# Optimization experiments

Measured on AMD Instinct MI355X. Metric: run time of the kernel, lower is better.

The kernel has to match this reference:

```python
import jax, jax.numpy as jnp
import numpy as np

N_NODES = 100000
N_EDGES = 1000000
D_FEAT = 64


def setup_inputs() -> dict:
    key = jax.random.key(0)
    k1, k2, k3, k4 = jax.random.split(key, 4)
    feat = jax.random.normal(k1, (N_NODES, D_FEAT), dtype=jnp.float32)
    edge_weight = jax.random.uniform(k2, (N_EDGES,), dtype=jnp.float32)
    edge_src = jax.random.randint(k3, (N_EDGES,), 0, N_NODES, dtype=jnp.int64)
    edge_dst = jax.random.randint(k4, (N_EDGES,), 0, N_NODES, dtype=jnp.int64)
    return {"feat": feat, "edge_weight": edge_weight,
            "edge_src": edge_src, "edge_dst": edge_dst}


def reference(feat, edge_weight, edge_src, edge_dst):
    # Original module reverses edges: graph((edges()[1], edges()[0])), then
    # u_mul_e('h','_edge_weight') + sum. So in terms of the ORIGINAL edge
    # orientation (edge_src -> edge_dst):
    #   out[edge_src] += feat[edge_dst] * edge_weight
    msgs = feat[edge_dst] * edge_weight[:, None]          # [E, D] gather + scale
    out = jax.ops.segment_sum(msgs, edge_src, num_segments=feat.shape[0])
    return out
```

## Files before the change

### kernel.cpp

```cpp
#include <hip/hip_runtime.h>


#define D_FEAT    64
#define SB        512
#define SB_SHIFT  9
#define CAPB      6144
#define BIN_CHUNK 4096
#define BIN_THR   512
#define CONV_BLK  512

typedef int      v2i __attribute__((ext_vector_type(2)));
typedef unsigned v4u __attribute__((ext_vector_type(4)));
typedef float    v4f __attribute__((ext_vector_type(4)));

__device__ __forceinline__ ushort f2bf(float f) {
    unsigned u = __float_as_uint(f);
    unsigned r = (u + 0x7fff + ((u >> 16) & 1)) >> 16;
    return (ushort)r;
}
__device__ __forceinline__ float bf_lo(unsigned u) { return __uint_as_float(u << 16); }
__device__ __forceinline__ float bf_hi(unsigned u) { return __uint_as_float(u & 0xffff0000u); }

__global__ __launch_bounds__(BIN_THR) void bin_conv(
    const float* __restrict__ feat, ushort* __restrict__ fh, int total4,
    const int* __restrict__ src, const int* __restrict__ dst,
    const float* __restrict__ w, int* __restrict__ cursor,
    long long* __restrict__ ep, int E, int NB, int nbin)
{
    if ((int)blockIdx.x >= nbin) {
        int cb = blockIdx.x - nbin;
        for (int i = cb * BIN_THR + threadIdx.x; i < total4; i += CONV_BLK * BIN_THR) {
            float4 v = reinterpret_cast<const float4*>(feat)[i];
            ushort4 o;
            o.x = f2bf(v.x); o.y = f2bf(v.y); o.z = f2bf(v.z); o.w = f2bf(v.w);
            reinterpret_cast<ushort4*>(fh)[i] = o;
        }
        return;
    }
    extern __shared__ int sh[];
    int* cnt   = sh;
    int* basel = sh + NB;
    int* stage = sh + 2 * NB;
    for (int b = threadIdx.x; b < NB; b += BIN_THR) cnt[b] = 0;
    __syncthreads();
    int start = blockIdx.x * BIN_CHUNK;
    int end   = min(start + BIN_CHUNK, E);
    for (int e = start + threadIdx.x; e < end; e += BIN_THR) {
        int s = src[e];
        int r = atomicAdd(&cnt[s >> SB_SHIFT], 1);
        stage[e - start] = s | (r << 17);
    }
    __syncthreads();
    for (int b = threadIdx.x; b < NB; b += BIN_THR) {
        int c = cnt[b];
        basel[b] = c ? atomicAdd(&cursor[b], c) : 0;
    }
    __syncthreads();
    for (int e = start + threadIdx.x; e < end; e += BIN_THR) {
        int sr = stage[e - start];
        int s  = sr & 0x1FFFF;
        int r  = (int)((unsigned)sr >> 17);
        int b  = s >> SB_SHIFT;
        int ls = s & (SB - 1);
        unsigned px = (unsigned)(dst[e] | (ls << 17));
        unsigned wb = __float_as_uint(w[e]);
        ep[(size_t)b * CAPB + basel[b] + r] =
            (long long)(((unsigned long long)wb << 32) | px);
    }
}

__global__ __launch_bounds__(1024) void node_sort(
    const int* __restrict__ cursor, long long* __restrict__ ep,
    v2i* __restrict__ node_rng, int N)
{
    __shared__ long long eb[CAPB];
    __shared__ ushort   rnk[CAPB];
    __shared__ int      cnt[SB];
    __shared__ int      wpre[8];
    int b = blockIdx.x, t = threadIdx.x;
    if (t < SB) cnt[t] = 0;
    __syncthreads();
    int sz = min(cursor[b], CAPB);
    int base = b * CAPB;
    for (int i = t; i < sz; i += 1024) {
        long long e = ep[base + i];
        eb[i] = e;
        int r = atomicAdd(&cnt[((int)(unsigned)e >> 17) & (SB - 1)], 1);
        rnk[i] = (ushort)r;
    }
    __syncthreads();
    int c = 0, x = 0;
    if (t < SB) {
        c = cnt[t];
        int lane = t & 63;
        x = c;
        #pragma unroll
        for (int d = 1; d < 64; d <<= 1) {
            int y = __shfl_up(x, d, 64);
            if (lane >= d) x += y;
        }
        if (lane == 63) wpre[t >> 6] = x;
    }
    __syncthreads();
    if (t == 0) {
        int run = 0;
        #pragma unroll
        for (int k = 0; k < 8; k++) { int v = wpre[k]; wpre[k] = run; run += v; }
    }
    __syncthreads();
    if (t < SB) {
        int excl = x - c + wpre[t >> 6];
        int node = b * SB + t;
        if (node < N) {
            v2i rng; rng.x = base + excl; rng.y = base + excl + c;
            node_rng[node] = rng;
        }
        cnt[t] = excl;
    }
    __syncthreads();
    for (int i = t; i < sz; i += 1024) {
        long long e = eb[i];
        unsigned px = (unsigned)e;
        int ls  = (int)(px >> 17) & (SB - 1);
        int pos = cnt[ls] + rnk[i];
        ep[base + pos] = (long long)((e & 0xffffffff00000000ull) | (px & 0x1FFFFu));
    }
}

__global__ __launch_bounds__(256) void segment_bf16(
    const ushort* __restrict__ fh, const v2i* __restrict__ node_rng,
    const long long* __restrict__ ep, float* __restrict__ out, int N)
{
    int tid  = blockIdx.x * blockDim.x + threadIdx.x;
    int node = tid >> 3;
    int q    = tid & 7;
    if (node >= N) return;
    v2i rng = node_rng[node];
    int j = rng.x, end = rng.y;
    float a0 = 0.f, a1 = 0.f, a2 = 0.f, a3 = 0.f;
    float a4 = 0.f, a5 = 0.f, a6 = 0.f, a7 = 0.f;
    for (; j + 4 <= end; j += 4) {
        long long e0 = ep[j],     e1 = ep[j + 1];
        long long e2 = ep[j + 2], e3 = ep[j + 3];
        v4u h0 = *reinterpret_cast<const v4u*>(&fh[(size_t)(unsigned)(e0 & 0x1FFFF) * D_FEAT + q * 8]);
        v4u h1 = *reinterpret_cast<const v4u*>(&fh[(size_t)(unsigned)(e1 & 0x1FFFF) * D_FEAT + q * 8]);
        v4u h2 = *reinterpret_cast<const v4u*>(&fh[(size_t)(unsigned)(e2 & 0x1FFFF) * D_FEAT + q * 8]);
        v4u h3 = *reinterpret_cast<const v4u*>(&fh[(size_t)(unsigned)(e3 & 0x1FFFF) * D_FEAT + q * 8]);
        float w0 = __uint_as_float((unsigned)((unsigned long long)e0 >> 32));
        float w1 = __uint_as_float((unsigned)((unsigned long long)e1 >> 32));
        float w2 = __uint_as_float((unsigned)((unsigned long long)e2 >> 32));
        float w3 = __uint_as_float((unsigned)((unsigned long long)e3 >> 32));
        a0 += bf_lo(h0.x) * w0; a1 += bf_hi(h0.x) * w0;
        a2 += bf_lo(h0.y) * w0; a3 += bf_hi(h0.y) * w0;
        a4 += bf_lo(h0.z) * w0; a5 += bf_hi(h0.z) * w0;
        a6 += bf_lo(h0.w) * w0; a7 += bf_hi(h0.w) * w0;
        a0 += bf_lo(h1.x) * w1; a1 += bf_hi(h1.x) * w1;
        a2 += bf_lo(h1.y) * w1; a3 += bf_hi(h1.y) * w1;
        a4 += bf_lo(h1.z) * w1; a5 += bf_hi(h1.z) * w1;
        a6 += bf_lo(h1.w) * w1; a7 += bf_hi(h1.w) * w1;
        a0 += bf_lo(h2.x) * w2; a1 += bf_hi(h2.x) * w2;
        a2 += bf_lo(h2.y) * w2; a3 += bf_hi(h2.y) * w2;
        a4 += bf_lo(h2.z) * w2; a5 += bf_hi(h2.z) * w2;
        a6 += bf_lo(h2.w) * w2; a7 += bf_hi(h2.w) * w2;
        a0 += bf_lo(h3.x) * w3; a1 += bf_hi(h3.x) * w3;
        a2 += bf_lo(h3.y) * w3; a3 += bf_hi(h3.y) * w3;
        a4 += bf_lo(h3.z) * w3; a5 += bf_hi(h3.z) * w3;
        a6 += bf_lo(h3.w) * w3; a7 += bf_hi(h3.w) * w3;
    }
    for (; j < end; j++) {
        long long e = ep[j];
        v4u h = *reinterpret_cast<const v4u*>(&fh[(size_t)(unsigned)(e & 0x1FFFF) * D_FEAT + q * 8]);
        float ww = __uint_as_float((unsigned)((unsigned long long)e >> 32));
        a0 += bf_lo(h.x) * ww; a1 += bf_hi(h.x) * ww;
        a2 += bf_lo(h.y) * ww; a3 += bf_hi(h.y) * ww;
        a4 += bf_lo(h.z) * ww; a5 += bf_hi(h.z) * ww;
        a6 += bf_lo(h.w) * ww; a7 += bf_hi(h.w) * ww;
    }
    float* o = &out[(size_t)node * D_FEAT + q * 8];
    *reinterpret_cast<v4f*>(o)     = v4f{a0, a1, a2, a3};
    *reinterpret_cast<v4f*>(o + 4) = v4f{a4, a5, a6, a7};
}

extern "C" void kernel_launch(void* const* d_in, const int* in_sizes, int n_in,
                              void* d_out, int out_size, void* d_ws, size_t ws_size,
                              hipStream_t stream) {
    const float* feat = (const float*)d_in[0];
    const float* w    = (const float*)d_in[1];
    const int*   src  = (const int*)d_in[2];
    const int*   dst  = (const int*)d_in[3];
    float* out = (float*)d_out;

    int N  = out_size / D_FEAT;
    int E  = in_sizes[1];
    int NB = (N + SB - 1) / SB;

    int* cursor   = (int*)d_ws;
    v2i* node_rng = (v2i*)(cursor + ((NB + 1) & ~1));
    uintptr_t ap = ((uintptr_t)(node_rng + N) + 15) & ~(uintptr_t)15;
    long long* ep = (long long*)ap;
    ushort* fh = (ushort*)(ep + (size_t)NB * CAPB);

    (void)hipMemsetAsync(cursor, 0, (size_t)NB * sizeof(int), stream);

    int nbin = (E + BIN_CHUNK - 1) / BIN_CHUNK;
    size_t lds_bin = (2 * (size_t)NB + BIN_CHUNK) * sizeof(int);
    int total4 = N * D_FEAT / 4;

    bin_conv<<<nbin + CONV_BLK, BIN_THR, lds_bin, stream>>>(
        feat, fh, total4, src, dst, w, cursor, ep, E, NB, nbin);
    node_sort<<<NB, 1024, 0, stream>>>(cursor, ep, node_rng, N);

    long long segthreads = (long long)N * 8;
    segment_bf16<<<(int)((segthreads + 255) / 256), 256, 0, stream>>>(
        fh, node_rng, ep, out, N);
}
```

Baseline: 71.91 us.

## Fuse per-bucket sort and segment reduction into one LDS-resident kernel

Merges the node_sort and segment_bf16 kernels into a single sort_seg kernel. Each block counting-sorts its bucket's edges into shared memory and then reduces them per node straight from LDS. The bucket size is halved to 256 nodes with a 3072-entry capacity so the sorted edges fit in shared memory. This drops the global write-back of sorted edges, the node_rng array and one kernel launch. In exchange there are fewer blocks (about 391) with 512 threads, and every wave runs 4 node rounds serially, which may cut latency hiding for the feature gathers.

```diff
diff --git a/kernel.cpp b/kernel.cpp
--- a/kernel.cpp
+++ b/kernel.cpp
@@ -2,14 +2,13 @@
 
 
 #define D_FEAT    64
-#define SB        512
-#define SB_SHIFT  9
-#define CAPB      6144
+#define SB        256
+#define SB_SHIFT  8
+#define CAPB      3072
 #define BIN_CHUNK 4096
 #define BIN_THR   512
 #define CONV_BLK  512
 
-typedef int      v2i __attribute__((ext_vector_type(2)));
 typedef unsigned v4u __attribute__((ext_vector_type(4)));
 typedef float    v4f __attribute__((ext_vector_type(4)));
 
@@ -69,31 +68,30 @@
     }
 }
 
-__global__ __launch_bounds__(1024) void node_sort(
-    const int* __restrict__ cursor, long long* __restrict__ ep,
-    v2i* __restrict__ node_rng, int N)
+__global__ __launch_bounds__(512) void sort_seg(
+    const int* __restrict__ cursor, const long long* __restrict__ ep,
+    const ushort* __restrict__ fh, float* __restrict__ out, int N)
 {
-    __shared__ long long eb[CAPB];
-    __shared__ ushort   rnk[CAPB];
-    __shared__ int      cnt[SB];
-    __shared__ int      wpre[8];
+    __shared__ unsigned long long es[CAPB];
+    __shared__ int cnt[SB];
+    __shared__ int nstart[SB];
+    __shared__ int cur[SB];
+    __shared__ int wpre[4];
     int b = blockIdx.x, t = threadIdx.x;
     if (t < SB) cnt[t] = 0;
     __syncthreads();
+    size_t base = (size_t)b * CAPB;
     int sz = min(cursor[b], CAPB);
-    int base = b * CAPB;
-    for (int i = t; i < sz; i += 1024) {
+    for (int i = t; i < sz; i += 512) {
         long long e = ep[base + i];
-        eb[i] = e;
-        int r = atomicAdd(&cnt[((int)(unsigned)e >> 17) & (SB - 1)], 1);
-        rnk[i] = (ushort)r;
+        atomicAdd(&cnt[((int)(unsigned)e >> 17) & (SB - 1)], 1);
     }
     __syncthreads();
     int c = 0, x = 0;
     if (t < SB) {
         c = cnt[t];
+        x = c;
         int lane = t & 63;
-        x = c;
         #pragma unroll
         for (int d = 1; d < 64; d <<= 1) {
             int y = __shfl_up(x, d, 64);
@@ -105,80 +103,74 @@
     if (t == 0) {
         int run = 0;
         #pragma unroll
-        for (int k = 0; k < 8; k++) { int v = wpre[k]; wpre[k] = run; run += v; }
+        for (int k = 0; k < 4; k++) { int v = wpre[k]; wpre[k] = run; run += v; }
     }
     __syncthreads();
     if (t < SB) {
         int excl = x - c + wpre[t >> 6];
-        int node = b * SB + t;
-        if (node < N) {
-            v2i rng; rng.x = base + excl; rng.y = base + excl + c;
-            node_rng[node] = rng;
-        }
-        cnt[t] = excl;
-    }
-    __syncthreads();
-    for (int i = t; i < sz; i += 1024) {
-        long long e = eb[i];
-        unsigned px = (unsigned)e;
-        int ls  = (int)(px >> 17) & (SB - 1);
-        int pos = cnt[ls] + rnk[i];
-        ep[base + pos] = (long long)((e & 0xffffffff00000000ull) | (px & 0x1FFFFu));
-    }
-}
-
-__global__ __launch_bounds__(256) void segment_bf16(
-    const ushort* __restrict__ fh, const v2i* __restrict__ node_rng,
-    const long long* __restrict__ ep, float* __restrict__ out, int N)
-{
-    int tid  = blockIdx.x * blockDim.x + threadIdx.x;
-    int node = tid >> 3;
-    int q    = tid & 7;
-    if (node >= N) return;
-    v2i rng = node_rng[node];
-    int j = rng.x, end = rng.y;
-    float a0 = 0.f, a1 = 0.f, a2 = 0.f, a3 = 0.f;
-    float a4 = 0.f, a5 = 0.f, a6 = 0.f, a7 = 0.f;
-    for (; j + 4 <= end; j += 4) {
-        long long e0 = ep[j],     e1 = ep[j + 1];
-        long long e2 = ep[j + 2], e3 = ep[j + 3];
-        v4u h0 = *reinterpret_cast<const v4u*>(&fh[(size_t)(unsigned)(e0 & 0x1FFFF) * D_FEAT + q * 8]);
-        v4u h1 = *reinterpret_cast<const v4u*>(&fh[(size_t)(unsigned)(e1 & 0x1FFFF) * D_FEAT + q * 8]);
-        v4u h2 = *reinterpret_cast<const v4u*>(&fh[(size_t)(unsigned)(e2 & 0x1FFFF) * D_FEAT + q * 8]);
-        v4u h3 = *reinterpret_cast<const v4u*>(&fh[(size_t)(unsigned)(e3 & 0x1FFFF) * D_FEAT + q * 8]);
-        float w0 = __uint_as_float((unsigned)((unsigned long long)e0 >> 32));
-        float w1 = __uint_as_float((unsigned)((unsigned long long)e1 >> 32));
-        float w2 = __uint_as_float((unsigned)((unsigned long long)e2 >> 32));
-        float w3 = __uint_as_float((unsigned)((unsigned long long)e3 >> 32));
-        a0 += bf_lo(h0.x) * w0; a1 += bf_hi(h0.x) * w0;
-        a2 += bf_lo(h0.y) * w0; a3 += bf_hi(h0.y) * w0;
-        a4 += bf_lo(h0.z) * w0; a5 += bf_hi(h0.z) * w0;
-        a6 += bf_lo(h0.w) * w0; a7 += bf_hi(h0.w) * w0;
-        a0 += bf_lo(h1.x) * w1; a1 += bf_hi(h1.x) * w1;
-        a2 += bf_lo(h1.y) * w1; a3 += bf_hi(h1.y) * w1;
-        a4 += bf_lo(h1.z) * w1; a5 += bf_hi(h1.z) * w1;
-        a6 += bf_lo(h1.w) * w1; a7 += bf_hi(h1.w) * w1;
-        a0 += bf_lo(h2.x) * w2; a1 += bf_hi(h2.x) * w2;
-        a2 += bf_lo(h2.y) * w2; a3 += bf_hi(h2.y) * w2;
-        a4 += bf_lo(h2.z) * w2; a5 += bf_hi(h2.z) * w2;
-        a6 += bf_lo(h2.w) * w2; a7 += bf_hi(h2.w) * w2;
-        a0 += bf_lo(h3.x) * w3; a1 += bf_hi(h3.x) * w3;
-        a2 += bf_lo(h3.y) * w3; a3 += bf_hi(h3.y) * w3;
-        a4 += bf_lo(h3.z) * w3; a5 += bf_hi(h3.z) * w3;
-        a6 += bf_lo(h3.w) * w3; a7 += bf_hi(h3.w) * w3;
-    }
-    for (; j < end; j++) {
-        long long e = ep[j];
-        v4u h = *reinterpret_cast<const v4u*>(&fh[(size_t)(unsigned)(e & 0x1FFFF) * D_FEAT + q * 8]);
-        float ww = __uint_as_float((unsigned)((unsigned long long)e >> 32));
-        a0 += bf_lo(h.x) * ww; a1 += bf_hi(h.x) * ww;
-        a2 += bf_lo(h.y) * ww; a3 += bf_hi(h.y) * ww;
-        a4 += bf_lo(h.z) * ww; a5 += bf_hi(h.z) * ww;
-        a6 += bf_lo(h.w) * ww; a7 += bf_hi(h.w) * ww;
-    }
-    float* o = &out[(size_t)node * D_FEAT + q * 8];
-    *reinterpret_cast<v4f*>(o)     = v4f{a0, a1, a2, a3};
-    *reinterpret_cast<v4f*>(o + 4) = v4f{a4, a5, a6, a7};
+        nstart[t] = excl;
+        cur[t]    = excl;
+        cnt[t]    = excl + c;
+    }
+    __syncthreads();
+    for (int i = t; i < sz; i += 512) {
+        long long e = ep[base + i];
+        int ls = ((int)(unsigned)e >> 17) & (SB - 1);
+        int pos = atomicAdd(&cur[ls], 1);
+        es[pos] = (unsigned long long)e;
+    }
+    __syncthreads();
+    #pragma unroll
+    for (int rd = 0; rd < 4; rd++) {
+        int local = rd * 64 + (t >> 3);
+        int q     = t & 7;
+        int node  = b * SB + local;
+        if (node >= N) continue;
+        int j   = nstart[local];
+        int end = cnt[local];
+        float a0 = 0.f, a1 = 0.f, a2 = 0.f, a3 = 0.f;
+        float a4 = 0.f, a5 = 0.f, a6 = 0.f, a7 = 0.f;
+        for (; j + 4 <= end; j += 4) {
+            unsigned long long e0 = es[j],     e1 = es[j + 1];
+            unsigned long long e2 = es[j + 2], e3 = es[j + 3];
+            v4u h0 = *reinterpret_cast<const v4u*>(&fh[(size_t)(unsigned)(e0 & 0x1FFFF) * D_FEAT + q * 8]);
+            v4u h1 = *reinterpret_cast<const v4u*>(&fh[(size_t)(unsigned)(e1 & 0x1FFFF) * D_FEAT + q * 8]);
+            v4u h2 = *reinterpret_cast<const v4u*>(&fh[(size_t)(unsigned)(e2 & 0x1FFFF) * D_FEAT + q * 8]);
+            v4u h3 = *reinterpret_cast<const v4u*>(&fh[(size_t)(unsigned)(e3 & 0x1FFFF) * D_FEAT + q * 8]);
+            float w0 = __uint_as_float((unsigned)(e0 >> 32));
+            float w1 = __uint_as_float((unsigned)(e1 >> 32));
+            float w2 = __uint_as_float((unsigned)(e2 >> 32));
+            float w3 = __uint_as_float((unsigned)(e3 >> 32));
+            a0 += bf_lo(h0.x) * w0; a1 += bf_hi(h0.x) * w0;
+            a2 += bf_lo(h0.y) * w0; a3 += bf_hi(h0.y) * w0;
+            a4 += bf_lo(h0.z) * w0; a5 += bf_hi(h0.z) * w0;
+            a6 += bf_lo(h0.w) * w0; a7 += bf_hi(h0.w) * w0;
+            a0 += bf_lo(h1.x) * w1; a1 += bf_hi(h1.x) * w1;
+            a2 += bf_lo(h1.y) * w1; a3 += bf_hi(h1.y) * w1;
+            a4 += bf_lo(h1.z) * w1; a5 += bf_hi(h1.z) * w1;
+            a6 += bf_lo(h1.w) * w1; a7 += bf_hi(h1.w) * w1;
+            a0 += bf_lo(h2.x) * w2; a1 += bf_hi(h2.x) * w2;
+            a2 += bf_lo(h2.y) * w2; a3 += bf_hi(h2.y) * w2;
+            a4 += bf_lo(h2.z) * w2; a5 += bf_hi(h2.z) * w2;
+            a6 += bf_lo(h2.w) * w2; a7 += bf_hi(h2.w) * w2;
+            a0 += bf_lo(h3.x) * w3; a1 += bf_hi(h3.x) * w3;
+            a2 += bf_lo(h3.y) * w3; a3 += bf_hi(h3.y) * w3;
+            a4 += bf_lo(h3.z) * w3; a5 += bf_hi(h3.z) * w3;
+            a6 += bf_lo(h3.w) * w3; a7 += bf_hi(h3.w) * w3;
+        }
+        for (; j < end; j++) {
+            unsigned long long e = es[j];
+            v4u h = *reinterpret_cast<const v4u*>(&fh[(size_t)(unsigned)(e & 0x1FFFF) * D_FEAT + q * 8]);
+            float ww = __uint_as_float((unsigned)(e >> 32));
+            a0 += bf_lo(h.x) * ww; a1 += bf_hi(h.x) * ww;
+            a2 += bf_lo(h.y) * ww; a3 += bf_hi(h.y) * ww;
+            a4 += bf_lo(h.z) * ww; a5 += bf_hi(h.z) * ww;
+            a6 += bf_lo(h.w) * ww; a7 += bf_hi(h.w) * ww;
+        }
+        float* o = &out[(size_t)node * D_FEAT + q * 8];
+        *reinterpret_cast<v4f*>(o)     = v4f{a0, a1, a2, a3};
+        *reinterpret_cast<v4f*>(o + 4) = v4f{a4, a5, a6, a7};
+    }
 }
 
 extern "C" void kernel_launch(void* const* d_in, const int* in_sizes, int n_in,
@@ -194,9 +186,8 @@
     int E  = in_sizes[1];
     int NB = (N + SB - 1) / SB;
 
-    int* cursor   = (int*)d_ws;
-    v2i* node_rng = (v2i*)(cursor + ((NB + 1) & ~1));
-    uintptr_t ap = ((uintptr_t)(node_rng + N) + 15) & ~(uintptr_t)15;
+    int* cursor = (int*)d_ws;
+    uintptr_t ap = ((uintptr_t)(cursor + NB) + 15) & ~(uintptr_t)15;
     long long* ep = (long long*)ap;
     ushort* fh = (ushort*)(ep + (size_t)NB * CAPB);
 
@@ -208,9 +199,5 @@
 
     bin_conv<<<nbin + CONV_BLK, BIN_THR, lds_bin, stream>>>(
         feat, fh, total4, src, dst, w, cursor, ep, E, NB, nbin);
-    node_sort<<<NB, 1024, 0, stream>>>(cursor, ep, node_rng, N);
-
-    long long segthreads = (long long)N * 8;
-    segment_bf16<<<(int)((segthreads + 255) / 256), 256, 0, stream>>>(
-        fh, node_rng, ep, out, N);
-}
+    sort_seg<<<NB, 512, 0, stream>>>(cursor, ep, fh, out, N);
+}
```

New measurement: 63.59 us. 1.13x faster.
